# Kernel tuning notes

Measured on AMD Instinct MI355X. Metric: run time of the kernel, lower is better.

Reference implementation:

```python
import jax, jax.numpy as jnp
import numpy as np

# Module config (matches init_kwargs)
SHAPE = (32, 32)          # wire grid
KERNEL = (3, 3)           # window per dim
NUM_LAYERS = 4
NINPUTS = int(np.prod(KERNEL))        # 9
NPOS = 2 ** NINPUTS                   # 512 possible boolean input combos


def _bitmask():
    # itertools.product(range(2), repeat=NINPUTS) then transpose -> (NINPUTS, NPOS)
    # combination j, window-element m has bit (j >> (NINPUTS-1-m)) & 1
    j = jnp.arange(NPOS)
    m = jnp.arange(NINPUTS)
    return ((j[None, :] >> (NINPUTS - 1 - m)[:, None]) & 1).astype(jnp.float32)


def _convolve(x):
    # x: (B, H, W) -> (B, H, W, K) wrapped sliding windows (im2col via rolls),
    # faithful to ASIC.convolve with kernel_offset='center'.
    out = x
    for d, k in enumerate(KERNEL):
        # window element i along dim d comes from position +i (wraparound)
        out = jnp.stack([jnp.roll(out, -i, axis=1 + d) for i in range(k)], axis=out.ndim)
    out = out.reshape(x.shape + (-1,))  # (B, H, W, K) with k0 slowest-varying
    # 'center' offset: roll by prod((k-1)//2) along the LAST spatial dim (as the torch code does)
    shift = int(np.prod([(k - 1) // 2 for k in KERNEL]))
    out = jnp.roll(out, shift, axis=len(KERNEL))  # axis = last spatial axis in (B, H, W, K)
    return out


def setup_inputs() -> dict:
    key = jax.random.key(0)
    k1, k2 = jax.random.split(key)
    x = jax.random.uniform(k1, (16,) + SHAPE, dtype=jnp.float32)
    toggle_gates = jax.random.uniform(k2, (NUM_LAYERS, NPOS) + SHAPE, dtype=jnp.float32)
    return {"x": x, "toggle_gates": toggle_gates}


def reference(x, toggle_gates):
    tw = jax.nn.sigmoid(toggle_gates)       # (L, NPOS, H, W)
    bits = _bitmask()                        # (NINPUTS, NPOS)
    # embed(): shape == x spatial shape -> stride-1 slices; initial state is x, output is full state
    state = x                                # (B, H, W)
    for layer in range(NUM_LAYERS):
        conv = _convolve(state)              # (B, H, W, K)
        # soft-LUT weights: prod over window elems of (1 - |bit - input|)
        w = jnp.prod(1.0 - jnp.abs(conv[..., None] - bits), axis=-2)  # (B, H, W, NPOS)
        state = jnp.clip(jnp.einsum('bhwp,phw->bhw', w, tw[layer]), 0.0, 1.0)
    return state
```

## Files before the change

### kernel.cpp

```cpp
#include <hip/hip_runtime.h>

#define HH 32
#define WW 32
#define NB 16
#define NPOS 512
#define TILE 8
#define PPAD 516

__global__ __launch_bounds__(128) void asic_layer(
    const float* __restrict__ src,
    const float* __restrict__ tg,
    float* __restrict__ dst)
{
    __shared__ float lut[TILE * PPAD];

    const int t    = threadIdx.x;
    const int hw0  = blockIdx.x * TILE;

    #pragma unroll
    for (int k = 0; k < 32; ++k) {
        int f   = t + 128 * k;
        int p   = f >> 3;
        int hwl = f & 7;
        float g = tg[p * (HH * WW) + hw0 + hwl];
        lut[hwl * PPAD + p] = 1.0f / (1.0f + __expf(-g));
    }
    __syncthreads();

    const int b   = t >> 3;
    const int hwl = t & 7;
    const int h   = hw0 >> 5;
    const int w   = (hw0 & 31) + hwl;

    float c[9];
    const float* sb = src + b * (HH * WW);
    #pragma unroll
    for (int i = 0; i < 3; ++i) {
        int row = ((h + i) & 31) * 32;
        #pragma unroll
        for (int j = 0; j < 3; ++j) {
            c[3 * i + j] = sb[row + ((w + j - 1 + 32) & 31)];
        }
    }

    float v[32];
    {
        float a2[2], a4[4], a8[8], a16[16];
        a2[0] = 1.0f - c[4]; a2[1] = c[4];
        #pragma unroll
        for (int q = 0; q < 2; ++q)  { a4[2*q]  = a2[q]  * (1.0f - c[5]); a4[2*q+1]  = a2[q]  * c[5]; }
        #pragma unroll
        for (int q = 0; q < 4; ++q)  { a8[2*q]  = a4[q]  * (1.0f - c[6]); a8[2*q+1]  = a4[q]  * c[6]; }
        #pragma unroll
        for (int q = 0; q < 8; ++q)  { a16[2*q] = a8[q]  * (1.0f - c[7]); a16[2*q+1] = a8[q]  * c[7]; }
        #pragma unroll
        for (int q = 0; q < 16; ++q) { v[2*q]   = a16[q] * (1.0f - c[8]); v[2*q+1]   = a16[q] * c[8]; }
    }
    float u[16];
    {
        float a2[2], a4[4], a8[8];
        a2[0] = 1.0f - c[0]; a2[1] = c[0];
        #pragma unroll
        for (int q = 0; q < 2; ++q) { a4[2*q] = a2[q] * (1.0f - c[1]); a4[2*q+1] = a2[q] * c[1]; }
        #pragma unroll
        for (int q = 0; q < 4; ++q) { a8[2*q] = a4[q] * (1.0f - c[2]); a8[2*q+1] = a4[q] * c[2]; }
        #pragma unroll
        for (int q = 0; q < 8; ++q) { u[2*q]  = a8[q] * (1.0f - c[3]); u[2*q+1]  = a8[q] * c[3]; }
    }

    const float4* lut4 = (const float4*)(lut + hwl * PPAD);
    float acc = 0.0f;
    #pragma unroll
    for (int hi = 0; hi < 16; ++hi) {
        float ps = 0.0f;
        #pragma unroll
        for (int l4 = 0; l4 < 8; ++l4) {
            float4 L = lut4[hi * 8 + l4];
            ps += L.x * v[4*l4] + L.y * v[4*l4+1] + L.z * v[4*l4+2] + L.w * v[4*l4+3];
        }
        acc += u[hi] * ps;
    }

    acc = fminf(fmaxf(acc, 0.0f), 1.0f);
    dst[b * (HH * WW) + h * 32 + w] = acc;
}

extern "C" void kernel_launch(void* const* d_in, const int* in_sizes, int n_in,
                              void* d_out, int out_size, void* d_ws, size_t ws_size,
                              hipStream_t stream) {
    const float* x  = (const float*)d_in[0];
    const float* tg = (const float*)d_in[1];
    float* out = (float*)d_out;
    float* ws  = (float*)d_ws;

    const int grid = (HH * WW) / TILE;
    const size_t L = (size_t)NPOS * HH * WW;

    asic_layer<<<grid, 128, 0, stream>>>(x,   tg + 0 * L, ws);
    asic_layer<<<grid, 128, 0, stream>>>(ws,  tg + 1 * L, out);
    asic_layer<<<grid, 128, 0, stream>>>(out, tg + 2 * L, ws);
    asic_layer<<<grid, 128, 0, stream>>>(ws,  tg + 3 * L, out);
}
```

Before: 85.28 us.

## Fuse four layer launches into one persistent kernel with grid barriers

Replaces four separate layer kernel launches with a single persistent kernel of 128 blocks. Blocks synchronise between layers through an atomic-counter grid barrier, and the barrier counters are reset with a memset before launch. Each layer's LUT sigmoid load is issued before its window loads and before the block barrier, so it overlaps with them, and the dot product is split into four independent FMA chains. This removes per-launch overhead and inter-kernel gaps. In exchange it relies on all blocks being co-resident and adds spin-wait cost plus a memset launch.

```diff
diff --git a/kernel.cpp b/kernel.cpp
--- a/kernel.cpp
+++ b/kernel.cpp
@@ -6,83 +6,114 @@
 #define NPOS 512
 #define TILE 8
 #define PPAD 516
+#define NBLK 128
+#define NLAYERS 4
 
-__global__ __launch_bounds__(128) void asic_layer(
-    const float* __restrict__ src,
+__device__ __forceinline__ void grid_barrier(int* cnt) {
+    __syncthreads();
+    if (threadIdx.x == 0) {
+        __threadfence();
+        __hip_atomic_fetch_add(cnt, 1, __ATOMIC_ACQ_REL, __HIP_MEMORY_SCOPE_AGENT);
+        while (__hip_atomic_load(cnt, __ATOMIC_ACQUIRE, __HIP_MEMORY_SCOPE_AGENT) < NBLK) {
+            __builtin_amdgcn_s_sleep(1);
+        }
+        __threadfence();
+    }
+    __syncthreads();
+}
+
+__global__ __launch_bounds__(128) void asic_fused(
+    const float* __restrict__ x,
     const float* __restrict__ tg,
-    float* __restrict__ dst)
+    float* __restrict__ bufA,
+    float* __restrict__ bufB,
+    float* __restrict__ out,
+    int* __restrict__ bar)
 {
     __shared__ float lut[TILE * PPAD];
 
-    const int t    = threadIdx.x;
-    const int hw0  = blockIdx.x * TILE;
-
-    #pragma unroll
-    for (int k = 0; k < 32; ++k) {
-        int f   = t + 128 * k;
-        int p   = f >> 3;
-        int hwl = f & 7;
-        float g = tg[p * (HH * WW) + hw0 + hwl];
-        lut[hwl * PPAD + p] = 1.0f / (1.0f + __expf(-g));
-    }
-    __syncthreads();
-
+    const int t   = threadIdx.x;
+    const int hw0 = blockIdx.x * TILE;
     const int b   = t >> 3;
     const int hwl = t & 7;
     const int h   = hw0 >> 5;
     const int w   = (hw0 & 31) + hwl;
 
-    float c[9];
-    const float* sb = src + b * (HH * WW);
-    #pragma unroll
-    for (int i = 0; i < 3; ++i) {
-        int row = ((h + i) & 31) * 32;
+    const float* src = x;
+
+    for (int layer = 0; layer < NLAYERS; ++layer) {
+        float* dst = (layer == 3) ? out : ((layer & 1) ? bufB : bufA);
+        const float* tgl = tg + (size_t)layer * NPOS * HH * WW;
+
         #pragma unroll
-        for (int j = 0; j < 3; ++j) {
-            c[3 * i + j] = sb[row + ((w + j - 1 + 32) & 31)];
+        for (int k = 0; k < 32; ++k) {
+            int f   = t + 128 * k;
+            int p   = f >> 3;
+            int pos = f & 7;
+            float g = tgl[p * (HH * WW) + hw0 + pos];
+            lut[pos * PPAD + p] = 1.0f / (1.0f + __expf(-g));
         }
+
+        float c[9];
+        const float* sb = src + b * (HH * WW);
+        #pragma unroll
+        for (int i = 0; i < 3; ++i) {
+            int row = ((h + i) & 31) * 32;
+            #pragma unroll
+            for (int j = 0; j < 3; ++j) {
+                c[3 * i + j] = sb[row + ((w + j - 1 + 32) & 31)];
+            }
+        }
+
+        __syncthreads();
+
+        float v[32];
+        {
+            float a2[2], a4[4], a8[8], a16[16];
+            a2[0] = 1.0f - c[4]; a2[1] = c[4];
+            #pragma unroll
+            for (int q = 0; q < 2; ++q)  { a4[2*q]  = a2[q]  * (1.0f - c[5]); a4[2*q+1]  = a2[q]  * c[5]; }
+            #pragma unroll
+            for (int q = 0; q < 4; ++q)  { a8[2*q]  = a4[q]  * (1.0f - c[6]); a8[2*q+1]  = a4[q]  * c[6]; }
+            #pragma unroll
+            for (int q = 0; q < 8; ++q)  { a16[2*q] = a8[q]  * (1.0f - c[7]); a16[2*q+1] = a8[q]  * c[7]; }
+            #pragma unroll
+            for (int q = 0; q < 16; ++q) { v[2*q]   = a16[q] * (1.0f - c[8]); v[2*q+1]   = a16[q] * c[8]; }
+        }
+        float u[16];
+        {
+            float a2[2], a4[4], a8[8];
+            a2[0] = 1.0f - c[0]; a2[1] = c[0];
+            #pragma unroll
+            for (int q = 0; q < 2; ++q) { a4[2*q] = a2[q] * (1.0f - c[1]); a4[2*q+1] = a2[q] * c[1]; }
+            #pragma unroll
+            for (int q = 0; q < 4; ++q) { a8[2*q] = a4[q] * (1.0f - c[2]); a8[2*q+1] = a4[q] * c[2]; }
+            #pragma unroll
+            for (int q = 0; q < 8; ++q) { u[2*q]  = a8[q] * (1.0f - c[3]); u[2*q+1]  = a8[q] * c[3]; }
+        }
+
+        const float4* lut4 = (const float4*)(lut + hwl * PPAD);
+        float acc = 0.0f;
+        #pragma unroll
+        for (int hi = 0; hi < 16; ++hi) {
+            float ps0 = 0.f, ps1 = 0.f, ps2 = 0.f, ps3 = 0.f;
+            #pragma unroll
+            for (int l4 = 0; l4 < 8; ++l4) {
+                float4 L = lut4[hi * 8 + l4];
+                ps0 = fmaf(L.x, v[4*l4+0], ps0);
+                ps1 = fmaf(L.y, v[4*l4+1], ps1);
+                ps2 = fmaf(L.z, v[4*l4+2], ps2);
+                ps3 = fmaf(L.w, v[4*l4+3], ps3);
+            }
+            acc = fmaf(u[hi], (ps0 + ps1) + (ps2 + ps3), acc);
+        }
+
+        acc = fminf(fmaxf(acc, 0.0f), 1.0f);
+        dst[b * (HH * WW) + h * 32 + w] = acc;
+
+        if (layer < NLAYERS - 1) grid_barrier(bar + layer);
+        src = dst;
     }
-
-    float v[32];
-    {
-        float a2[2], a4[4], a8[8], a16[16];
-        a2[0] = 1.0f - c[4]; a2[1] = c[4];
-        #pragma unroll
-        for (int q = 0; q < 2; ++q)  { a4[2*q]  = a2[q]  * (1.0f - c[5]); a4[2*q+1]  = a2[q]  * c[5]; }
-        #pragma unroll
-        for (int q = 0; q < 4; ++q)  { a8[2*q]  = a4[q]  * (1.0f - c[6]); a8[2*q+1]  = a4[q]  * c[6]; }
-        #pragma unroll
-        for (int q = 0; q < 8; ++q)  { a16[2*q] = a8[q]  * (1.0f - c[7]); a16[2*q+1] = a8[q]  * c[7]; }
-        #pragma unroll
-        for (int q = 0; q < 16; ++q) { v[2*q]   = a16[q] * (1.0f - c[8]); v[2*q+1]   = a16[q] * c[8]; }
-    }
-    float u[16];
-    {
-        float a2[2], a4[4], a8[8];
-        a2[0] = 1.0f - c[0]; a2[1] = c[0];
-        #pragma unroll
-        for (int q = 0; q < 2; ++q) { a4[2*q] = a2[q] * (1.0f - c[1]); a4[2*q+1] = a2[q] * c[1]; }
-        #pragma unroll
-        for (int q = 0; q < 4; ++q) { a8[2*q] = a4[q] * (1.0f - c[2]); a8[2*q+1] = a4[q] * c[2]; }
-        #pragma unroll
-        for (int q = 0; q < 8; ++q) { u[2*q]  = a8[q] * (1.0f - c[3]); u[2*q+1]  = a8[q] * c[3]; }
-    }
-
-    const float4* lut4 = (const float4*)(lut + hwl * PPAD);
-    float acc = 0.0f;
-    #pragma unroll
-    for (int hi = 0; hi < 16; ++hi) {
-        float ps = 0.0f;
-        #pragma unroll
-        for (int l4 = 0; l4 < 8; ++l4) {
-            float4 L = lut4[hi * 8 + l4];
-            ps += L.x * v[4*l4] + L.y * v[4*l4+1] + L.z * v[4*l4+2] + L.w * v[4*l4+3];
-        }
-        acc += u[hi] * ps;
-    }
-
-    acc = fminf(fmaxf(acc, 0.0f), 1.0f);
-    dst[b * (HH * WW) + h * 32 + w] = acc;
 }
 
 extern "C" void kernel_launch(void* const* d_in, const int* in_sizes, int n_in,
@@ -90,14 +121,11 @@
                               hipStream_t stream) {
     const float* x  = (const float*)d_in[0];
     const float* tg = (const float*)d_in[1];
-    float* out = (float*)d_out;
-    float* ws  = (float*)d_ws;
+    float* out  = (float*)d_out;
+    float* bufA = (float*)d_ws;
+    float* bufB = bufA + NB * HH * WW;
+    int*   bar  = (int*)((char*)d_ws + 256 * 1024);
 
-    const int grid = (HH * WW) / TILE;
-    const size_t L = (size_t)NPOS * HH * WW;
-
-    asic_layer<<<grid, 128, 0, stream>>>(x,   tg + 0 * L, ws);
-    asic_layer<<<grid, 128, 0, stream>>>(ws,  tg + 1 * L, out);
-    asic_layer<<<grid, 128, 0, stream>>>(out, tg + 2 * L, ws);
-    asic_layer<<<grid, 128, 0, stream>>>(ws,  tg + 3 * L, out);
+    hipMemsetAsync(bar, 0, 4 * sizeof(int), stream);
+    asic_fused<<<NBLK, 128, 0, stream>>>(x, tg, bufA, bufB, out, bar);
 }
```

Measured after the change: 112.3 us. +31.6%, slower.

## Split LUT dot product across 4 thread groups with shared-memory reduction

Applied to the files above, without the earlier changes.

Blocks grow from 128 to 512 threads. Each group of 128 threads handles a quarter of the 512-entry LUT contraction, and the partial sums are reduced through shared memory before the clamp and store. The sigmoid LUT load is also spread over four times as many threads, the window loads now happen before the barrier, and the inner accumulation uses four independent FMA chains. This aims to raise parallelism and hide latency on a grid of only 128 blocks, at the cost of an extra barrier and redundant computation of the window products in every group.

```diff
diff --git a/kernel.cpp b/kernel.cpp
--- a/kernel.cpp
+++ b/kernel.cpp
@@ -6,83 +6,98 @@
 #define NPOS 512
 #define TILE 8
 #define PPAD 516
+#define NTHR 512
 
-__global__ __launch_bounds__(128) void asic_layer(
+__global__ __launch_bounds__(NTHR) void asic_layer(
     const float* __restrict__ src,
     const float* __restrict__ tg,
     float* __restrict__ dst)
 {
     __shared__ float lut[TILE * PPAD];
+    __shared__ float red[NTHR];
 
-    const int t    = threadIdx.x;
-    const int hw0  = blockIdx.x * TILE;
+    const int t   = threadIdx.x;
+    const int hw0 = blockIdx.x * TILE;
 
     #pragma unroll
-    for (int k = 0; k < 32; ++k) {
-        int f   = t + 128 * k;
+    for (int k = 0; k < 8; ++k) {
+        int f   = t + NTHR * k;
         int p   = f >> 3;
-        int hwl = f & 7;
-        float g = tg[p * (HH * WW) + hw0 + hwl];
-        lut[hwl * PPAD + p] = 1.0f / (1.0f + __expf(-g));
+        int pos = f & 7;
+        float g = tg[p * (HH * WW) + hw0 + pos];
+        lut[pos * PPAD + p] = 1.0f / (1.0f + __expf(-g));
     }
-    __syncthreads();
 
-    const int b   = t >> 3;
-    const int hwl = t & 7;
+    const int c   = t & 127;
+    const int q   = t >> 7;
+    const int b   = c >> 3;
+    const int hwl = c & 7;
     const int h   = hw0 >> 5;
     const int w   = (hw0 & 31) + hwl;
 
-    float c[9];
+    float cc[9];
     const float* sb = src + b * (HH * WW);
     #pragma unroll
     for (int i = 0; i < 3; ++i) {
         int row = ((h + i) & 31) * 32;
         #pragma unroll
         for (int j = 0; j < 3; ++j) {
-            c[3 * i + j] = sb[row + ((w + j - 1 + 32) & 31)];
+            cc[3 * i + j] = sb[row + ((w + j - 1 + 32) & 31)];
         }
     }
+
+    __syncthreads();
 
     float v[32];
     {
         float a2[2], a4[4], a8[8], a16[16];
-        a2[0] = 1.0f - c[4]; a2[1] = c[4];
+        a2[0] = 1.0f - cc[4]; a2[1] = cc[4];
         #pragma unroll
-        for (int q = 0; q < 2; ++q)  { a4[2*q]  = a2[q]  * (1.0f - c[5]); a4[2*q+1]  = a2[q]  * c[5]; }
+        for (int i = 0; i < 2; ++i)  { a4[2*i]  = a2[i]  * (1.0f - cc[5]); a4[2*i+1]  = a2[i]  * cc[5]; }
         #pragma unroll
-        for (int q = 0; q < 4; ++q)  { a8[2*q]  = a4[q]  * (1.0f - c[6]); a8[2*q+1]  = a4[q]  * c[6]; }
+        for (int i = 0; i < 4; ++i)  { a8[2*i]  = a4[i]  * (1.0f - cc[6]); a8[2*i+1]  = a4[i]  * cc[6]; }
         #pragma unroll
-        for (int q = 0; q < 8; ++q)  { a16[2*q] = a8[q]  * (1.0f - c[7]); a16[2*q+1] = a8[q]  * c[7]; }
+        for (int i = 0; i < 8; ++i)  { a16[2*i] = a8[i]  * (1.0f - cc[7]); a16[2*i+1] = a8[i]  * cc[7]; }
         #pragma unroll
-        for (int q = 0; q < 16; ++q) { v[2*q]   = a16[q] * (1.0f - c[8]); v[2*q+1]   = a16[q] * c[8]; }
+        for (int i = 0; i < 16; ++i) { v[2*i]   = a16[i] * (1.0f - cc[8]); v[2*i+1]   = a16[i] * cc[8]; }
     }
     float u[16];
     {
         float a2[2], a4[4], a8[8];
-        a2[0] = 1.0f - c[0]; a2[1] = c[0];
+        a2[0] = 1.0f - cc[0]; a2[1] = cc[0];
         #pragma unroll
-        for (int q = 0; q < 2; ++q) { a4[2*q] = a2[q] * (1.0f - c[1]); a4[2*q+1] = a2[q] * c[1]; }
+        for (int i = 0; i < 2; ++i) { a4[2*i] = a2[i] * (1.0f - cc[1]); a4[2*i+1] = a2[i] * cc[1]; }
         #pragma unroll
-        for (int q = 0; q < 4; ++q) { a8[2*q] = a4[q] * (1.0f - c[2]); a8[2*q+1] = a4[q] * c[2]; }
+        for (int i = 0; i < 4; ++i) { a8[2*i] = a4[i] * (1.0f - cc[2]); a8[2*i+1] = a4[i] * cc[2]; }
         #pragma unroll
-        for (int q = 0; q < 8; ++q) { u[2*q]  = a8[q] * (1.0f - c[3]); u[2*q+1]  = a8[q] * c[3]; }
+        for (int i = 0; i < 8; ++i) { u[2*i]  = a8[i] * (1.0f - cc[3]); u[2*i+1]  = a8[i] * cc[3]; }
     }
 
     const float4* lut4 = (const float4*)(lut + hwl * PPAD);
     float acc = 0.0f;
     #pragma unroll
-    for (int hi = 0; hi < 16; ++hi) {
-        float ps = 0.0f;
+    for (int hh = 0; hh < 4; ++hh) {
+        int hi = 4 * q + hh;
+        float ps0 = 0.f, ps1 = 0.f, ps2 = 0.f, ps3 = 0.f;
         #pragma unroll
         for (int l4 = 0; l4 < 8; ++l4) {
             float4 L = lut4[hi * 8 + l4];
-            ps += L.x * v[4*l4] + L.y * v[4*l4+1] + L.z * v[4*l4+2] + L.w * v[4*l4+3];
+            ps0 = fmaf(L.x, v[4*l4+0], ps0);
+            ps1 = fmaf(L.y, v[4*l4+1], ps1);
+            ps2 = fmaf(L.z, v[4*l4+2], ps2);
+            ps3 = fmaf(L.w, v[4*l4+3], ps3);
         }
-        acc += u[hi] * ps;
+        acc = fmaf(u[hi], (ps0 + ps1) + (ps2 + ps3), acc);
     }
 
-    acc = fminf(fmaxf(acc, 0.0f), 1.0f);
-    dst[b * (HH * WW) + h * 32 + w] = acc;
+    red[t] = acc;
+    __syncthreads();
+
+    if (t < 128) {
+        float s = (red[t] + red[t + 128]) + (red[t + 256] + red[t + 384]);
+        s = fminf(fmaxf(s, 0.0f), 1.0f);
+        dst[b * (HH * WW) + h * 32 + w] = s;
+    }
 }
 
 extern "C" void kernel_launch(void* const* d_in, const int* in_sizes, int n_in,
@@ -96,8 +111,8 @@
     const int grid = (HH * WW) / TILE;
     const size_t L = (size_t)NPOS * HH * WW;
 
-    asic_layer<<<grid, 128, 0, stream>>>(x,   tg + 0 * L, ws);
-    asic_layer<<<grid, 128, 0, stream>>>(ws,  tg + 1 * L, out);
-    asic_layer<<<grid, 128, 0, stream>>>(out, tg + 2 * L, ws);
-    asic_layer<<<grid, 128, 0, stream>>>(ws,  tg + 3 * L, out);
+    asic_layer<<<grid, NTHR, 0, stream>>>(x,   tg + 0 * L, ws);
+    asic_layer<<<grid, NTHR, 0, stream>>>(ws,  tg + 1 * L, out);
+    asic_layer<<<grid, NTHR, 0, stream>>>(out, tg + 2 * L, ws);
+    asic_layer<<<grid, NTHR, 0, stream>>>(ws,  tg + 3 * L, out);
 }
```

Result: faster. 78.30 us (-8.2%).

## Fuse pairs of layers into one kernel with halo recomputation of first layer

Applied to the files above, without the earlier changes.

Merges two consecutive ASIC layers into a single kernel. Each block recomputes the first layer over a 3x10 halo of 30 positions, keeping the intermediate state in shared memory, then evaluates the second layer for its 8-position tile. This halves the launch count and drops the global round trip for the intermediate state. The cost is about 3.75x redundant first-layer work and LUT loads, plus a larger block, more shared memory and more registers per thread. Work is split across batch halves, with cross-lane shuffles and shared-memory reductions over the LUT high bits.

```diff
diff --git a/kernel.cpp b/kernel.cpp
--- a/kernel.cpp
+++ b/kernel.cpp
@@ -2,87 +2,193 @@
 
 #define HH 32
 #define WW 32
-#define NB 16
 #define NPOS 512
 #define TILE 8
-#define PPAD 516
-
-__global__ __launch_bounds__(128) void asic_layer(
+#define NTHR 512
+#define HSTR 36
+#define PSTR 580
+#define NPA 30
+#define NPB 8
+#define RSTR 132
+
+__device__ __forceinline__ void make_v(const float c[9], float* v) {
+    float a2[2], a4[4], a8[8], a16[16];
+    a2[0] = 1.0f - c[4]; a2[1] = c[4];
+    #pragma unroll
+    for (int i = 0; i < 2; ++i)  { a4[2*i]  = a2[i]  * (1.0f - c[5]); a4[2*i+1]  = a2[i]  * c[5]; }
+    #pragma unroll
+    for (int i = 0; i < 4; ++i)  { a8[2*i]  = a4[i]  * (1.0f - c[6]); a8[2*i+1]  = a4[i]  * c[6]; }
+    #pragma unroll
+    for (int i = 0; i < 8; ++i)  { a16[2*i] = a8[i]  * (1.0f - c[7]); a16[2*i+1] = a8[i]  * c[7]; }
+    #pragma unroll
+    for (int i = 0; i < 16; ++i) { v[2*i]   = a16[i] * (1.0f - c[8]); v[2*i+1]   = a16[i] * c[8]; }
+}
+
+__global__ __launch_bounds__(NTHR, 2) void asic_pair(
     const float* __restrict__ src,
-    const float* __restrict__ tg,
+    const float* __restrict__ tgA,
+    const float* __restrict__ tgB,
     float* __restrict__ dst)
 {
-    __shared__ float lut[TILE * PPAD];
-
-    const int t    = threadIdx.x;
-    const int hw0  = blockIdx.x * TILE;
-
-    #pragma unroll
-    for (int k = 0; k < 32; ++k) {
-        int f   = t + 128 * k;
-        int p   = f >> 3;
-        int hwl = f & 7;
-        float g = tg[p * (HH * WW) + hw0 + hwl];
-        lut[hwl * PPAD + p] = 1.0f / (1.0f + __expf(-g));
-    }
+    __shared__ float lutA[NPA * PSTR];
+    __shared__ float lutB[NPB * PSTR];
+    __shared__ float mid[NPA * 8];
+    __shared__ float redB[NPB * RSTR];
+
+    const int t     = threadIdx.x;
+    const int sp    = blockIdx.x & 127;
+    const int bhalf = blockIdx.x >> 7;
+    const int hw0   = sp * TILE;
+    const int h     = hw0 >> 5;
+    const int w0    = hw0 & 31;
+
+    #pragma unroll 5
+    for (int k = 0; k < NPA; ++k) {
+        unsigned f = t + NTHR * k;
+        unsigned p = f / 30u;
+        unsigned pos = f - 30u * p;
+        unsigned i  = pos / 10u;
+        unsigned jj = pos - 10u * i;
+        int rm = (h + (int)i) & 31;
+        int cm = (w0 - 1 + (int)jj + 32) & 31;
+        float g = tgA[p * (HH * WW) + rm * 32 + cm];
+        lutA[pos * PSTR + (p >> 5) * HSTR + (p & 31)] = 1.0f / (1.0f + __expf(-g));
+    }
+    #pragma unroll 4
+    for (int k = 0; k < NPB; ++k) {
+        unsigned f = t + NTHR * k;
+        unsigned p  = f >> 3;
+        unsigned pb = f & 7;
+        float g = tgB[p * (HH * WW) + h * 32 + (w0 + (int)pb)];
+        lutB[pb * PSTR + (p >> 5) * HSTR + (p & 31)] = 1.0f / (1.0f + __expf(-g));
+    }
+
+    const int hs  = t & 7;
+    const int bg  = (t >> 3) & 1;
+    const int pos = t >> 4;
+    const unsigned ip  = (unsigned)pos / 10u;
+    const unsigned jjp = (unsigned)pos - 10u * ip;
+    const int rmA  = h + (int)ip;
+    const int cmbA = w0 - 1 + (int)jjp;
+    const int b0   = bhalf * 8 + bg * 4;
+
+    const int m0 = (hs >> 2) & 1, m1 = (hs >> 1) & 1, m2 = hs & 1;
+
+    float vA[4][32], ubase[4], c3v[4];
+    #pragma unroll
+    for (int bb = 0; bb < 4; ++bb) {
+        const float* sb = src + (size_t)(b0 + bb) * (HH * WW);
+        float c[9];
+        #pragma unroll
+        for (int ii = 0; ii < 3; ++ii) {
+            int row = ((rmA + ii) & 31) * 32;
+            #pragma unroll
+            for (int ji = 0; ji < 3; ++ji) {
+                c[3 * ii + ji] = sb[row + ((cmbA + ji - 1 + 32) & 31)];
+            }
+        }
+        make_v(c, vA[bb]);
+        float f0 = m0 ? c[0] : 1.0f - c[0];
+        float f1 = m1 ? c[1] : 1.0f - c[1];
+        float f2 = m2 ? c[2] : 1.0f - c[2];
+        ubase[bb] = f0 * f1 * f2;
+        c3v[bb]   = c[3];
+    }
+
     __syncthreads();
 
-    const int b   = t >> 3;
-    const int hwl = t & 7;
-    const int h   = hw0 >> 5;
-    const int w   = (hw0 & 31) + hwl;
-
-    float c[9];
-    const float* sb = src + b * (HH * WW);
-    #pragma unroll
-    for (int i = 0; i < 3; ++i) {
-        int row = ((h + i) & 31) * 32;
-        #pragma unroll
-        for (int j = 0; j < 3; ++j) {
-            c[3 * i + j] = sb[row + ((w + j - 1 + 32) & 31)];
-        }
-    }
-
-    float v[32];
+    float acc[4] = {0.f, 0.f, 0.f, 0.f};
     {
-        float a2[2], a4[4], a8[8], a16[16];
-        a2[0] = 1.0f - c[4]; a2[1] = c[4];
-        #pragma unroll
-        for (int q = 0; q < 2; ++q)  { a4[2*q]  = a2[q]  * (1.0f - c[5]); a4[2*q+1]  = a2[q]  * c[5]; }
-        #pragma unroll
-        for (int q = 0; q < 4; ++q)  { a8[2*q]  = a4[q]  * (1.0f - c[6]); a8[2*q+1]  = a4[q]  * c[6]; }
-        #pragma unroll
-        for (int q = 0; q < 8; ++q)  { a16[2*q] = a8[q]  * (1.0f - c[7]); a16[2*q+1] = a8[q]  * c[7]; }
-        #pragma unroll
-        for (int q = 0; q < 16; ++q) { v[2*q]   = a16[q] * (1.0f - c[8]); v[2*q+1]   = a16[q] * c[8]; }
-    }
-    float u[16];
+        const float* baseA = lutA + pos * PSTR + (2 * hs) * HSTR;
+        #pragma unroll
+        for (int hp = 0; hp < 2; ++hp) {
+            const float4* L4 = (const float4*)(baseA + hp * HSTR);
+            float ps[4] = {0.f, 0.f, 0.f, 0.f};
+            #pragma unroll
+            for (int l4 = 0; l4 < 8; ++l4) {
+                float4 L = L4[l4];
+                #pragma unroll
+                for (int bb = 0; bb < 4; ++bb) {
+                    ps[bb] = fmaf(L.x, vA[bb][4*l4+0], ps[bb]);
+                    ps[bb] = fmaf(L.y, vA[bb][4*l4+1], ps[bb]);
+                    ps[bb] = fmaf(L.z, vA[bb][4*l4+2], ps[bb]);
+                    ps[bb] = fmaf(L.w, vA[bb][4*l4+3], ps[bb]);
+                }
+            }
+            #pragma unroll
+            for (int bb = 0; bb < 4; ++bb) {
+                float u = ubase[bb] * (hp ? c3v[bb] : (1.0f - c3v[bb]));
+                acc[bb] = fmaf(u, ps[bb], acc[bb]);
+            }
+        }
+    }
+    #pragma unroll
+    for (int mask = 1; mask <= 4; mask <<= 1) {
+        #pragma unroll
+        for (int bb = 0; bb < 4; ++bb) acc[bb] += __shfl_xor(acc[bb], mask, 64);
+    }
+    if (hs == 0 && pos < NPA) {
+        float4 m4;
+        m4.x = fminf(fmaxf(acc[0], 0.0f), 1.0f);
+        m4.y = fminf(fmaxf(acc[1], 0.0f), 1.0f);
+        m4.z = fminf(fmaxf(acc[2], 0.0f), 1.0f);
+        m4.w = fminf(fmaxf(acc[3], 0.0f), 1.0f);
+        *(float4*)(mid + pos * 8 + bg * 4) = m4;
+    }
+    __syncthreads();
+
     {
-        float a2[2], a4[4], a8[8];
-        a2[0] = 1.0f - c[0]; a2[1] = c[0];
-        #pragma unroll
-        for (int q = 0; q < 2; ++q) { a4[2*q] = a2[q] * (1.0f - c[1]); a4[2*q+1] = a2[q] * c[1]; }
-        #pragma unroll
-        for (int q = 0; q < 4; ++q) { a8[2*q] = a4[q] * (1.0f - c[2]); a8[2*q+1] = a4[q] * c[2]; }
-        #pragma unroll
-        for (int q = 0; q < 8; ++q) { u[2*q]  = a8[q] * (1.0f - c[3]); u[2*q+1]  = a8[q] * c[3]; }
-    }
-
-    const float4* lut4 = (const float4*)(lut + hwl * PPAD);
-    float acc = 0.0f;
-    #pragma unroll
-    for (int hi = 0; hi < 16; ++hi) {
-        float ps = 0.0f;
+        const int posB = t >> 6;
+        const int bp   = (t >> 4) & 3;
+        const int hi   = t & 15;
+
+        float c0[9], c1[9];
+        #pragma unroll
+        for (int wi = 0; wi < 3; ++wi) {
+            #pragma unroll
+            for (int wj = 0; wj < 3; ++wj) {
+                float2 m = *(const float2*)(mid + (wi * 10 + posB + wj) * 8 + bp * 2);
+                c0[3 * wi + wj] = m.x;
+                c1[3 * wi + wj] = m.y;
+            }
+        }
+        float v0[32], v1[32];
+        make_v(c0, v0);
+        make_v(c1, v1);
+
+        const int hm0 = (hi >> 3) & 1, hm1 = (hi >> 2) & 1, hm2 = (hi >> 1) & 1, hm3 = hi & 1;
+        float u0 = (hm0 ? c0[0] : 1.0f - c0[0]) * (hm1 ? c0[1] : 1.0f - c0[1])
+                 * (hm2 ? c0[2] : 1.0f - c0[2]) * (hm3 ? c0[3] : 1.0f - c0[3]);
+        float u1 = (hm0 ? c1[0] : 1.0f - c1[0]) * (hm1 ? c1[1] : 1.0f - c1[1])
+                 * (hm2 ? c1[2] : 1.0f - c1[2]) * (hm3 ? c1[3] : 1.0f - c1[3]);
+
+        const float4* L4 = (const float4*)(lutB + posB * PSTR + hi * HSTR);
+        float p0a = 0.f, p0b = 0.f, p1a = 0.f, p1b = 0.f;
         #pragma unroll
         for (int l4 = 0; l4 < 8; ++l4) {
-            float4 L = lut4[hi * 8 + l4];
-            ps += L.x * v[4*l4] + L.y * v[4*l4+1] + L.z * v[4*l4+2] + L.w * v[4*l4+3];
-        }
-        acc += u[hi] * ps;
-    }
-
-    acc = fminf(fmaxf(acc, 0.0f), 1.0f);
-    dst[b * (HH * WW) + h * 32 + w] = acc;
+            float4 L = L4[l4];
+            p0a = fmaf(L.x, v0[4*l4+0], p0a); p0a = fmaf(L.y, v0[4*l4+1], p0a);
+            p0b = fmaf(L.z, v0[4*l4+2], p0b); p0b = fmaf(L.w, v0[4*l4+3], p0b);
+            p1a = fmaf(L.x, v1[4*l4+0], p1a); p1a = fmaf(L.y, v1[4*l4+1], p1a);
+            p1b = fmaf(L.z, v1[4*l4+2], p1b); p1b = fmaf(L.w, v1[4*l4+3], p1b);
+        }
+        float2 r;
+        r.x = u0 * (p0a + p0b);
+        r.y = u1 * (p1a + p1b);
+        *(float2*)(redB + posB * RSTR + hi * 8 + bp * 2) = r;
+    }
+    __syncthreads();
+
+    if (t < 64) {
+        int posB = t >> 3;
+        int bl   = t & 7;
+        const float* rb = redB + posB * RSTR + bl;
+        float s = 0.0f;
+        #pragma unroll
+        for (int hi = 0; hi < 16; ++hi) s += rb[hi * 8];
+        s = fminf(fmaxf(s, 0.0f), 1.0f);
+        dst[(size_t)(bhalf * 8 + bl) * (HH * WW) + h * 32 + (w0 + posB)] = s;
+    }
 }
 
 extern "C" void kernel_launch(void* const* d_in, const int* in_sizes, int n_in,
@@ -93,11 +199,9 @@
     float* out = (float*)d_out;
     float* ws  = (float*)d_ws;
 
-    const int grid = (HH * WW) / TILE;
+    const int grid = 256;
     const size_t L = (size_t)NPOS * HH * WW;
 
-    asic_layer<<<grid, 128, 0, stream>>>(x,   tg + 0 * L, ws);
-    asic_layer<<<grid, 128, 0, stream>>>(ws,  tg + 1 * L, out);
-    asic_layer<<<grid, 128, 0, stream>>>(out, tg + 2 * L, ws);
-    asic_layer<<<grid, 128, 0, stream>>>(ws,  tg + 3 * L, out);
+    asic_pair<<<grid, NTHR, 0, stream>>>(x,  tg + 0 * L, tg + 1 * L, ws);
+    asic_pair<<<grid, NTHR, 0, stream>>>(ws, tg + 2 * L, tg + 3 * L, out);
 }
```

Result: faster. 81.80 us (-4.1%).
